# Kernel optimization log

Measured on AMD Instinct MI355X. Metric: run time of the kernel, lower is better.

Reference implementation:

```python
import jax, jax.numpy as jnp
import numpy as np

B, N, E = 16, 5000, 160000
IN, OUT, H = 64, 64, 1  # heads=1 (GATConv default)
NEG_SLOPE = 0.2


def setup_inputs() -> dict:
    key = jax.random.key(0)
    ks = jax.random.split(key, 10)
    data = jax.random.normal(ks[0], (B, N, IN), jnp.float32)
    # random edges with no self-loops (PyG removes then re-adds self-loops;
    # with no pre-existing self-loops this matches exactly)
    src = jax.random.randint(ks[1], (E,), 0, N)
    off = jax.random.randint(ks[2], (E,), 1, N)
    dst = (src + off) % N
    edge_index = jnp.stack([src, dst]).astype(jnp.int32)
    edge_attr = jax.random.uniform(ks[3], (E,), jnp.float32)
    # GATConv parameters (glorot-ish init)
    W = jax.random.normal(ks[4], (H * OUT, IN), jnp.float32) / np.sqrt(IN)
    W_edge = jax.random.normal(ks[5], (H * OUT, 1), jnp.float32)
    att_src = jax.random.normal(ks[6], (1, H, OUT), jnp.float32) * 0.1
    att_dst = jax.random.normal(ks[7], (1, H, OUT), jnp.float32) * 0.1
    att_edge = jax.random.normal(ks[8], (1, H, OUT), jnp.float32) * 0.1
    bias = jnp.zeros((H * OUT,), jnp.float32)
    return {"data": data, "edge_index": edge_index, "edge_attr": edge_attr,
            "W": W, "W_edge": W_edge, "att_src": att_src, "att_dst": att_dst,
            "att_edge": att_edge, "bias": bias}


def reference(data, edge_index, edge_attr, W, W_edge, att_src, att_dst, att_edge, bias):
    BN = B * N
    x = data.reshape(BN, IN)
    # faithful to source: tile edges per batch WITHOUT node offset
    ei = jnp.tile(edge_index, (1, B))          # [2, B*E]
    ea = jnp.tile(edge_attr, B)[:, None]        # [B*E, 1]
    # add self-loops for all BN nodes, edge_attr filled with mean
    loops = jnp.arange(BN, dtype=ei.dtype)
    src = jnp.concatenate([ei[0], loops])       # [Etot]
    dst = jnp.concatenate([ei[1], loops])
    ea = jnp.concatenate([ea, jnp.full((BN, 1), ea.mean(), ea.dtype)])
    # linear transforms
    xl = (x @ W.T).reshape(BN, H, OUT)          # [BN, H, C]
    a_src = (xl * att_src).sum(-1)              # [BN, H]
    a_dst = (xl * att_dst).sum(-1)
    e_emb = (ea @ W_edge.T).reshape(-1, H, OUT) # [Etot, H, C]
    a_edge = (e_emb * att_edge).sum(-1)         # [Etot, H]
    # per-edge attention + segment softmax over destination nodes
    alpha = a_src[src] + a_dst[dst] + a_edge
    alpha = jax.nn.leaky_relu(alpha, NEG_SLOPE)
    amax = jax.ops.segment_max(alpha, dst, num_segments=BN)
    alpha = jnp.exp(alpha - amax[dst])
    denom = jax.ops.segment_sum(alpha, dst, num_segments=BN)
    alpha = alpha / (denom[dst] + 1e-16)
    # message passing: gather src features, weight, scatter-sum to dst
    msg = xl[src] * alpha[:, :, None]           # [Etot, H, C]
    out = jax.ops.segment_sum(msg, dst, num_segments=BN)
    out = out.reshape(BN, H * OUT) + bias
    return out.reshape(B, N, OUT), jnp.stack([src, dst]), alpha
```

## Files before the change

### kernel.cpp

```cpp
#include <hip/hip_runtime.h>

#define NN 5000
#define EE 160000
#define BB 16
#define BNN 80000
#define BEE 2560000
#define ETOT 2640000
#define CAP 128
#define POISON ((int)0xAAAAAAAA)

#define GEMM_BLKS 1250
#define SUM_BLKS  80
#define OUT1_BLKS 2578
#define FILL_BLKS 625
#define MEGA_BLKS (GEMM_BLKS + SUM_BLKS + OUT1_BLKS + FILL_BLKS)

typedef __attribute__((ext_vector_type(8))) short short8;
typedef __attribute__((ext_vector_type(4))) float floatx4;

__device__ __forceinline__ short8 pack_bf8(const float* p) {
    union { unsigned int u[4]; short8 s; } r;
    #pragma unroll
    for (int j = 0; j < 4; ++j) {
        unsigned int lo = __float_as_uint(p[2 * j]) >> 16;
        unsigned int hi = __float_as_uint(p[2 * j + 1]) & 0xFFFF0000u;
        r.u[j] = lo | hi;
    }
    return r.s;
}

__global__ __launch_bounds__(256) void k_mega(
        const float* __restrict__ x, const float* __restrict__ W,
        const float* __restrict__ att_src, const float* __restrict__ att_dst,
        const float* __restrict__ bias,
        const float* __restrict__ ea, const float* __restrict__ wedge,
        const float* __restrict__ atte, const int* __restrict__ ei,
        float* __restrict__ xl, float* __restrict__ asrc, float* __restrict__ adst,
        float* __restrict__ out0,
        int* __restrict__ cursor, int* __restrict__ bucket,
        float* __restrict__ partials, float* __restrict__ out1) {
    __shared__ float red[256];
    const int blk = blockIdx.x;
    const int t = threadIdx.x;

    if (blk < GEMM_BLKS) {
        const int wave = t >> 6;
        const int lane = t & 63;
        const int quad = lane >> 4;
        const int col  = lane & 15;
        short8 bfrag[4][2];
        float attsv[4], attdv[4], biasv[4];
        #pragma unroll
        for (int ct = 0; ct < 4; ++ct) {
            int c = ct * 16 + col;
            #pragma unroll
            for (int ks = 0; ks < 2; ++ks)
                bfrag[ct][ks] = pack_bf8(W + c * 64 + ks * 32 + quad * 8);
            attsv[ct] = att_src[c];
            attdv[ct] = att_dst[c];
            biasv[ct] = bias[c];
        }
        int node0 = (blk * 4 + wave) << 4;
        short8 afrag[2];
        const float* xrow = x + (size_t)(node0 + col) * 64;
        #pragma unroll
        for (int ks = 0; ks < 2; ++ks)
            afrag[ks] = pack_bf8(xrow + ks * 32 + quad * 8);
        floatx4 acc[4];
        #pragma unroll
        for (int ct = 0; ct < 4; ++ct) acc[ct] = (floatx4){0.f, 0.f, 0.f, 0.f};
        #pragma unroll
        for (int ks = 0; ks < 2; ++ks)
            #pragma unroll
            for (int ct = 0; ct < 4; ++ct)
                acc[ct] = __builtin_amdgcn_mfma_f32_16x16x32_bf16(afrag[ks], bfrag[ct][ks], acc[ct], 0, 0, 0);
        float ps[4] = {0.f,0.f,0.f,0.f}, pd[4] = {0.f,0.f,0.f,0.f};
        #pragma unroll
        for (int r = 0; r < 4; ++r) {
            int node = node0 + quad * 4 + r;
            #pragma unroll
            for (int ct = 0; ct < 4; ++ct) {
                float v = acc[ct][r];
                out0[node * 64 + ct * 16 + col] = v + biasv[ct];
                if (node < NN) xl[node * 64 + ct * 16 + col] = v;
                ps[r] += v * attsv[ct];
                pd[r] += v * attdv[ct];
            }
        }
        #pragma unroll
        for (int off = 1; off < 16; off <<= 1) {
            #pragma unroll
            for (int r = 0; r < 4; ++r) {
                ps[r] += __shfl_xor(ps[r], off, 64);
                pd[r] += __shfl_xor(pd[r], off, 64);
            }
        }
        if (col == 0) {
            #pragma unroll
            for (int r = 0; r < 4; ++r) {
                int node = node0 + quad * 4 + r;
                if (node < NN) { asrc[node] = ps[r]; adst[node] = pd[r]; }
            }
        }
    } else if (blk < GEMM_BLKS + SUM_BLKS) {
        int sb = blk - GEMM_BLKS;
        int gid = sb * 256 + t;
        float v = 0.f;
        for (int i = gid; i < EE; i += SUM_BLKS * 256) v += ea[i];
        red[t] = v;
        __syncthreads();
        #pragma unroll
        for (int off = 128; off > 0; off >>= 1) {
            if (t < off) red[t] += red[t + off];
            __syncthreads();
        }
        if (t == 0) partials[sb] = red[0];
        if (sb == 0 && t < 64) {
            float s = wedge[t] * atte[t];
            #pragma unroll
            for (int off = 32; off > 0; off >>= 1) s += __shfl_xor(s, off, 64);
            if (t == 0) partials[80] = s;
        }
    } else if (blk < GEMM_BLKS + SUM_BLKS + OUT1_BLKS) {
        int qb = blk - (GEMM_BLKS + SUM_BLKS);
        for (int q = qb * 256 + t; q < ETOT / 4; q += OUT1_BLKS * 256) {
            int i = q * 4;
            float4 sv, dv;
            if (i < BEE) {
                int oe = i % EE;
                int4 s4 = *reinterpret_cast<const int4*>(ei + oe);
                int4 d4 = *reinterpret_cast<const int4*>(ei + EE + oe);
                sv = make_float4((float)s4.x, (float)s4.y, (float)s4.z, (float)s4.w);
                dv = make_float4((float)d4.x, (float)d4.y, (float)d4.z, (float)d4.w);
            } else {
                int nn = i - BEE;
                sv = make_float4((float)nn, (float)(nn+1), (float)(nn+2), (float)(nn+3));
                dv = sv;
            }
            *reinterpret_cast<float4*>(out1 + i) = sv;
            *reinterpret_cast<float4*>(out1 + ETOT + i) = dv;
        }
    } else {
        int fb = blk - (GEMM_BLKS + SUM_BLKS + OUT1_BLKS);
        int e = fb * 256 + t;
        int d = ei[EE + e];
        int pos = atomicAdd(&cursor[d], 1) - POISON;
        if (pos < CAP) bucket[d * CAP + pos] = e;
    }
}

__global__ __launch_bounds__(256) void k_gather(
        const int* __restrict__ ei, const float* __restrict__ ea,
        const int* __restrict__ bucket, const int* __restrict__ cursor,
        const float* __restrict__ asrc, const float* __restrict__ adst,
        const float* __restrict__ partials,
        const float* __restrict__ xl, const float* __restrict__ bias,
        float* __restrict__ albuf, float* __restrict__ selfal,
        float* __restrict__ out0) {
    __shared__ float s_r[4][CAP];
    __shared__ int   s_se[4][CAP];
    __shared__ int   s_e[4][CAP];
    int wave = threadIdx.x >> 6, lane = threadIdx.x & 63;
    int d = blockIdx.x * 4 + wave;
    int deg = min(cursor[d] - POISON, CAP);
    float s0 = 0.f;
    #pragma unroll
    for (int i = 0; i < 80; ++i) s0 += partials[i];
    float s1 = partials[80];
    float mean = s0 * (1.0f / EE);
    float ad = adst[d];
    float rs = asrc[d] + ad + mean * s1;
    rs = (rs > 0.f) ? rs : 0.2f * rs;
    float rmax = rs;
    for (int base = 0; base < deg; base += 64) {
        int idx = base + lane;
        if (idx < deg) {
            int e  = bucket[d * CAP + idx];
            int se = ei[e];
            float r = asrc[se] + ad + ea[e] * s1;
            r = (r > 0.f) ? r : 0.2f * r;
            s_r[wave][idx] = r; s_se[wave][idx] = se; s_e[wave][idx] = e;
            rmax = fmaxf(rmax, r);
        }
    }
    #pragma unroll
    for (int off = 32; off > 0; off >>= 1) rmax = fmaxf(rmax, __shfl_xor(rmax, off, 64));
    float m = rmax;
    float es = __expf(rs - m);
    float l = es;
    float acc = es * xl[d * 64 + lane];
    int j = 0;
    for (; j + 4 <= deg; j += 4) {
        int se0 = s_se[wave][j],     se1 = s_se[wave][j + 1];
        int se2 = s_se[wave][j + 2], se3 = s_se[wave][j + 3];
        float x0 = xl[se0 * 64 + lane], x1 = xl[se1 * 64 + lane];
        float x2 = xl[se2 * 64 + lane], x3 = xl[se3 * 64 + lane];
        float w0 = __expf(s_r[wave][j]     - m), w1 = __expf(s_r[wave][j + 1] - m);
        float w2 = __expf(s_r[wave][j + 2] - m), w3 = __expf(s_r[wave][j + 3] - m);
        acc += 16.0f * (w0 * x0 + w1 * x1 + w2 * x2 + w3 * x3);
        l   += 16.0f * (w0 + w1 + w2 + w3);
    }
    for (; j < deg; ++j) {
        int se0 = s_se[wave][j];
        float w0 = __expf(s_r[wave][j] - m);
        acc += 16.0f * w0 * xl[se0 * 64 + lane];
        l   += 16.0f * w0;
    }
    float inv = 1.0f / (l + 1e-16f);
    out0[d * 64 + lane] = acc * inv + bias[lane];
    if (lane == 0) selfal[d] = es * inv;
    for (int idx = lane; idx < deg; idx += 64)
        albuf[s_e[wave][idx]] = __expf(s_r[wave][idx] - m) * inv;
}

__global__ void k_alpha(const float* __restrict__ albuf,
                        const float* __restrict__ selfal,
                        float* __restrict__ out2) {
    int t = threadIdx.x;
    for (int q = blockIdx.x * 256 + t; q < ETOT / 4; q += OUT1_BLKS * 256) {
        int i = q * 4;
        float4 av;
        if (i < BEE) {
            av = *reinterpret_cast<const float4*>(albuf + (i % EE));
        } else {
            float a[4];
            #pragma unroll
            for (int jj = 0; jj < 4; ++jj) {
                int nn = i + jj - BEE;
                a[jj] = (nn < NN) ? selfal[nn] : 1.0f;
            }
            av = make_float4(a[0], a[1], a[2], a[3]);
        }
        *reinterpret_cast<float4*>(out2 + i) = av;
    }
}

extern "C" void kernel_launch(void* const* d_in, const int* in_sizes, int n_in,
                              void* d_out, int out_size, void* d_ws, size_t ws_size,
                              hipStream_t stream) {
    const float* data  = (const float*)d_in[0];
    const int*   ei    = (const int*)d_in[1];
    const float* ea    = (const float*)d_in[2];
    const float* W     = (const float*)d_in[3];
    const float* wedge = (const float*)d_in[4];
    const float* atts  = (const float*)d_in[5];
    const float* attd  = (const float*)d_in[6];
    const float* atte  = (const float*)d_in[7];
    const float* bias  = (const float*)d_in[8];

    float* out0 = (float*)d_out;
    float* out1 = out0 + 5120000;
    float* out2 = out0 + 10400000;

    float* ws = (float*)d_ws;
    float* xl       = ws;
    float* asrc     = ws + 320000;
    float* adst     = ws + 325000;
    float* albuf    = ws + 330000;
    float* selfal   = ws + 490000;
    float* partials = ws + 495000;
    int*   cursor   = (int*)(ws + 495082);
    int*   bucket   = (int*)(ws + 500082);

    k_mega  <<<MEGA_BLKS, 256, 0, stream>>>(data, W, atts, attd, bias, ea, wedge,
                                            atte, ei, xl, asrc, adst, out0,
                                            cursor, bucket, partials, out1);
    k_gather<<<1250,      256, 0, stream>>>(ei, ea, bucket, cursor, asrc, adst,
                                            partials, xl, bias, albuf, selfal, out0);
    k_alpha <<<OUT1_BLKS, 256, 0, stream>>>(albuf, selfal, out2);
}
```

Baseline: 127.5 us.

## Rebalance kernel stages: move high-node GEMM and index output into gather kernel

Measured after the change: 130.1 us. +2.1%, slower.

```diff
diff --git a/kernel.cpp b/kernel.cpp
--- a/kernel.cpp
+++ b/kernel.cpp
@@ -2,18 +2,23 @@
 
 #define NN 5000
 #define EE 160000
-#define BB 16
 #define BNN 80000
 #define BEE 2560000
 #define ETOT 2640000
 #define CAP 128
 #define POISON ((int)0xAAAAAAAA)
 
-#define GEMM_BLKS 1250
-#define SUM_BLKS  80
-#define OUT1_BLKS 2578
-#define FILL_BLKS 625
-#define MEGA_BLKS (GEMM_BLKS + SUM_BLKS + OUT1_BLKS + FILL_BLKS)
+#define K1_FILL 625
+#define K1_GEMM 79
+#define K1_SUM  80
+#define K1_BLKS (K1_FILL + K1_GEMM + K1_SUM)
+
+#define K2_GATHER 1250
+#define K2_GEMMHI 1172
+#define K2_OUT1   2578
+#define K2_BLKS   (K2_GATHER + K2_GEMMHI + K2_OUT1)
+
+#define K3_BLKS 1290
 
 typedef __attribute__((ext_vector_type(8))) short short8;
 typedef __attribute__((ext_vector_type(4))) float floatx4;
@@ -29,84 +34,113 @@
     return r.s;
 }
 
-__global__ __launch_bounds__(256) void k_mega(
+template <bool LO>
+__device__ __forceinline__ void gemm_tile(
+        int gblk, int t,
         const float* __restrict__ x, const float* __restrict__ W,
         const float* __restrict__ att_src, const float* __restrict__ att_dst,
         const float* __restrict__ bias,
+        float* __restrict__ xl, float* __restrict__ asrc, float* __restrict__ adst,
+        float* __restrict__ out0) {
+    const int wave = t >> 6;
+    const int lane = t & 63;
+    const int quad = lane >> 4;
+    const int col  = lane & 15;
+    short8 bfrag[4][2];
+    float attsv[4], attdv[4], biasv[4];
+    #pragma unroll
+    for (int ct = 0; ct < 4; ++ct) {
+        int c = ct * 16 + col;
+        #pragma unroll
+        for (int ks = 0; ks < 2; ++ks)
+            bfrag[ct][ks] = pack_bf8(W + c * 64 + ks * 32 + quad * 8);
+        if (LO) { attsv[ct] = att_src[c]; attdv[ct] = att_dst[c]; }
+        else    { biasv[ct] = bias[c]; }
+    }
+    int node0 = (gblk * 4 + wave) << 4;
+    short8 afrag[2];
+    const float* xrow = x + (size_t)(node0 + col) * 64;
+    #pragma unroll
+    for (int ks = 0; ks < 2; ++ks)
+        afrag[ks] = pack_bf8(xrow + ks * 32 + quad * 8);
+    floatx4 acc[4];
+    #pragma unroll
+    for (int ct = 0; ct < 4; ++ct) acc[ct] = (floatx4){0.f, 0.f, 0.f, 0.f};
+    #pragma unroll
+    for (int ks = 0; ks < 2; ++ks)
+        #pragma unroll
+        for (int ct = 0; ct < 4; ++ct)
+            acc[ct] = __builtin_amdgcn_mfma_f32_16x16x32_bf16(afrag[ks], bfrag[ct][ks], acc[ct], 0, 0, 0);
+    if (LO) {
+        float ps[4] = {0.f,0.f,0.f,0.f}, pd[4] = {0.f,0.f,0.f,0.f};
+        #pragma unroll
+        for (int r = 0; r < 4; ++r) {
+            int node = node0 + quad * 4 + r;
+            #pragma unroll
+            for (int ct = 0; ct < 4; ++ct) {
+                float v = acc[ct][r];
+                if (node < NN) xl[node * 64 + ct * 16 + col] = v;
+                ps[r] += v * attsv[ct];
+                pd[r] += v * attdv[ct];
+            }
+        }
+        #pragma unroll
+        for (int off = 1; off < 16; off <<= 1) {
+            #pragma unroll
+            for (int r = 0; r < 4; ++r) {
+                ps[r] += __shfl_xor(ps[r], off, 64);
+                pd[r] += __shfl_xor(pd[r], off, 64);
+            }
+        }
+        if (col == 0) {
+            #pragma unroll
+            for (int r = 0; r < 4; ++r) {
+                int node = node0 + quad * 4 + r;
+                if (node < NN) { asrc[node] = ps[r]; adst[node] = pd[r]; }
+            }
+        }
+    } else {
+        #pragma unroll
+        for (int r = 0; r < 4; ++r) {
+            int node = node0 + quad * 4 + r;
+            #pragma unroll
+            for (int ct = 0; ct < 4; ++ct) {
+                float v = acc[ct][r];
+                if (node >= NN) out0[node * 64 + ct * 16 + col] = v + biasv[ct];
+            }
+        }
+    }
+}
+
+__global__ __launch_bounds__(256) void k1(
+        const float* __restrict__ x, const float* __restrict__ W,
+        const float* __restrict__ att_src, const float* __restrict__ att_dst,
         const float* __restrict__ ea, const float* __restrict__ wedge,
         const float* __restrict__ atte, const int* __restrict__ ei,
         float* __restrict__ xl, float* __restrict__ asrc, float* __restrict__ adst,
-        float* __restrict__ out0,
-        int* __restrict__ cursor, int* __restrict__ bucket,
-        float* __restrict__ partials, float* __restrict__ out1) {
+        int* __restrict__ cursor, int* __restrict__ bucket, float* __restrict__ eabuf,
+        float* __restrict__ partials) {
     __shared__ float red[256];
     const int blk = blockIdx.x;
     const int t = threadIdx.x;
-
-    if (blk < GEMM_BLKS) {
-        const int wave = t >> 6;
-        const int lane = t & 63;
-        const int quad = lane >> 4;
-        const int col  = lane & 15;
-        short8 bfrag[4][2];
-        float attsv[4], attdv[4], biasv[4];
-        #pragma unroll
-        for (int ct = 0; ct < 4; ++ct) {
-            int c = ct * 16 + col;
-            #pragma unroll
-            for (int ks = 0; ks < 2; ++ks)
-                bfrag[ct][ks] = pack_bf8(W + c * 64 + ks * 32 + quad * 8);
-            attsv[ct] = att_src[c];
-            attdv[ct] = att_dst[c];
-            biasv[ct] = bias[c];
-        }
-        int node0 = (blk * 4 + wave) << 4;
-        short8 afrag[2];
-        const float* xrow = x + (size_t)(node0 + col) * 64;
-        #pragma unroll
-        for (int ks = 0; ks < 2; ++ks)
-            afrag[ks] = pack_bf8(xrow + ks * 32 + quad * 8);
-        floatx4 acc[4];
-        #pragma unroll
-        for (int ct = 0; ct < 4; ++ct) acc[ct] = (floatx4){0.f, 0.f, 0.f, 0.f};
-        #pragma unroll
-        for (int ks = 0; ks < 2; ++ks)
-            #pragma unroll
-            for (int ct = 0; ct < 4; ++ct)
-                acc[ct] = __builtin_amdgcn_mfma_f32_16x16x32_bf16(afrag[ks], bfrag[ct][ks], acc[ct], 0, 0, 0);
-        float ps[4] = {0.f,0.f,0.f,0.f}, pd[4] = {0.f,0.f,0.f,0.f};
-        #pragma unroll
-        for (int r = 0; r < 4; ++r) {
-            int node = node0 + quad * 4 + r;
-            #pragma unroll
-            for (int ct = 0; ct < 4; ++ct) {
-                float v = acc[ct][r];
-                out0[node * 64 + ct * 16 + col] = v + biasv[ct];
-                if (node < NN) xl[node * 64 + ct * 16 + col] = v;
-                ps[r] += v * attsv[ct];
-                pd[r] += v * attdv[ct];
-            }
-        }
-        #pragma unroll
-        for (int off = 1; off < 16; off <<= 1) {
-            #pragma unroll
-            for (int r = 0; r < 4; ++r) {
-                ps[r] += __shfl_xor(ps[r], off, 64);
-                pd[r] += __shfl_xor(pd[r], off, 64);
-            }
-        }
-        if (col == 0) {
-            #pragma unroll
-            for (int r = 0; r < 4; ++r) {
-                int node = node0 + quad * 4 + r;
-                if (node < NN) { asrc[node] = ps[r]; adst[node] = pd[r]; }
-            }
-        }
-    } else if (blk < GEMM_BLKS + SUM_BLKS) {
-        int sb = blk - GEMM_BLKS;
+    if (blk < K1_FILL) {
+        int e = blk * 256 + t;
+        int s = ei[e];
+        int d = ei[EE + e];
+        float ev = ea[e];
+        int pos = atomicAdd(&cursor[d], 1) - POISON;
+        if (pos < CAP) {
+            bucket[d * CAP + pos] = (s << 18) | e;
+            eabuf[d * CAP + pos] = ev;
+        }
+    } else if (blk < K1_FILL + K1_GEMM) {
+        gemm_tile<true>(blk - K1_FILL, t, x, W, att_src, att_dst, nullptr,
+                        xl, asrc, adst, nullptr);
+    } else {
+        int sb = blk - (K1_FILL + K1_GEMM);
         int gid = sb * 256 + t;
         float v = 0.f;
-        for (int i = gid; i < EE; i += SUM_BLKS * 256) v += ea[i];
+        for (int i = gid; i < EE; i += K1_SUM * 256) v += ea[i];
         red[t] = v;
         __syncthreads();
         #pragma unroll
@@ -121,9 +155,85 @@
             for (int off = 32; off > 0; off >>= 1) s += __shfl_xor(s, off, 64);
             if (t == 0) partials[80] = s;
         }
-    } else if (blk < GEMM_BLKS + SUM_BLKS + OUT1_BLKS) {
-        int qb = blk - (GEMM_BLKS + SUM_BLKS);
-        for (int q = qb * 256 + t; q < ETOT / 4; q += OUT1_BLKS * 256) {
+    }
+}
+
+__global__ __launch_bounds__(256) void k2(
+        const float* __restrict__ x, const float* __restrict__ W,
+        const float* __restrict__ bias,
+        const int* __restrict__ ei,
+        const int* __restrict__ bucket, const float* __restrict__ eabuf,
+        const int* __restrict__ cursor,
+        const float* __restrict__ asrc, const float* __restrict__ adst,
+        const float* __restrict__ partials,
+        const float* __restrict__ xl,
+        float* __restrict__ albuf, float* __restrict__ selfal,
+        float* __restrict__ out0, float* __restrict__ out1) {
+    __shared__ float s_r[4][CAP];
+    __shared__ int   s_se[4][CAP];
+    __shared__ int   s_e[4][CAP];
+    const int blk = blockIdx.x;
+    const int t = threadIdx.x, w = t >> 6, lane = t & 63;
+
+    if (blk < K2_GATHER) {
+        float s0 = 0.f;
+        #pragma unroll
+        for (int i = 0; i < 80; ++i) s0 += partials[i];
+        float s1 = partials[80];
+        float selfadd = s0 * (1.0f / EE) * s1;
+        float bl = bias[lane];
+        int d = blk * 4 + w;
+        float* sr = s_r[w]; int* sse = s_se[w]; int* se_ = s_e[w];
+        int deg = min(cursor[d] - POISON, CAP);
+        float ad = adst[d];
+        float rs = asrc[d] + ad + selfadd;
+        rs = (rs > 0.f) ? rs : 0.2f * rs;
+        float rmax = rs;
+        for (int base = 0; base < deg; base += 64) {
+            int idx = base + lane;
+            if (idx < deg) {
+                int packed = bucket[d * CAP + idx];
+                float ev   = eabuf[d * CAP + idx];
+                int se = packed >> 18;
+                int e  = packed & 0x3FFFF;
+                float r = asrc[se] + ad + ev * s1;
+                r = (r > 0.f) ? r : 0.2f * r;
+                sr[idx] = r; sse[idx] = se; se_[idx] = e;
+                rmax = fmaxf(rmax, r);
+            }
+        }
+        #pragma unroll
+        for (int off = 32; off > 0; off >>= 1) rmax = fmaxf(rmax, __shfl_xor(rmax, off, 64));
+        float m = rmax;
+        float es = __expf(rs - m);
+        float l = es;
+        float acc = es * xl[d * 64 + lane];
+        int j = 0;
+        for (; j + 4 <= deg; j += 4) {
+            int a0 = sse[j], a1 = sse[j + 1], a2 = sse[j + 2], a3 = sse[j + 3];
+            float x0 = xl[a0 * 64 + lane], x1 = xl[a1 * 64 + lane];
+            float x2 = xl[a2 * 64 + lane], x3 = xl[a3 * 64 + lane];
+            float w0 = __expf(sr[j] - m),     w1 = __expf(sr[j + 1] - m);
+            float w2 = __expf(sr[j + 2] - m), w3 = __expf(sr[j + 3] - m);
+            acc += 16.0f * (w0 * x0 + w1 * x1 + w2 * x2 + w3 * x3);
+            l   += 16.0f * (w0 + w1 + w2 + w3);
+        }
+        for (; j < deg; ++j) {
+            float w0 = __expf(sr[j] - m);
+            acc += 16.0f * w0 * xl[sse[j] * 64 + lane];
+            l   += 16.0f * w0;
+        }
+        float inv = 1.0f / (l + 1e-16f);
+        out0[d * 64 + lane] = acc * inv + bl;
+        if (lane == 0) selfal[d] = es * inv;
+        for (int idx = lane; idx < deg; idx += 64)
+            albuf[se_[idx]] = __expf(sr[idx] - m) * inv;
+    } else if (blk < K2_GATHER + K2_GEMMHI) {
+        gemm_tile<false>(78 + (blk - K2_GATHER), t, x, W, nullptr, nullptr, bias,
+                         nullptr, nullptr, nullptr, out0);
+    } else {
+        int qb = blk - (K2_GATHER + K2_GEMMHI);
+        for (int q = qb * 256 + t; q < ETOT / 4; q += K2_OUT1 * 256) {
             int i = q * 4;
             float4 sv, dv;
             if (i < BEE) {
@@ -140,84 +250,13 @@
             *reinterpret_cast<float4*>(out1 + i) = sv;
             *reinterpret_cast<float4*>(out1 + ETOT + i) = dv;
         }
-    } else {
-        int fb = blk - (GEMM_BLKS + SUM_BLKS + OUT1_BLKS);
-        int e = fb * 256 + t;
-        int d = ei[EE + e];
-        int pos = atomicAdd(&cursor[d], 1) - POISON;
-        if (pos < CAP) bucket[d * CAP + pos] = e;
-    }
-}
-
-__global__ __launch_bounds__(256) void k_gather(
-        const int* __restrict__ ei, const float* __restrict__ ea,
-        const int* __restrict__ bucket, const int* __restrict__ cursor,
-        const float* __restrict__ asrc, const float* __restrict__ adst,
-        const float* __restrict__ partials,
-        const float* __restrict__ xl, const float* __restrict__ bias,
-        float* __restrict__ albuf, float* __restrict__ selfal,
-        float* __restrict__ out0) {
-    __shared__ float s_r[4][CAP];
-    __shared__ int   s_se[4][CAP];
-    __shared__ int   s_e[4][CAP];
-    int wave = threadIdx.x >> 6, lane = threadIdx.x & 63;
-    int d = blockIdx.x * 4 + wave;
-    int deg = min(cursor[d] - POISON, CAP);
-    float s0 = 0.f;
-    #pragma unroll
-    for (int i = 0; i < 80; ++i) s0 += partials[i];
-    float s1 = partials[80];
-    float mean = s0 * (1.0f / EE);
-    float ad = adst[d];
-    float rs = asrc[d] + ad + mean * s1;
-    rs = (rs > 0.f) ? rs : 0.2f * rs;
-    float rmax = rs;
-    for (int base = 0; base < deg; base += 64) {
-        int idx = base + lane;
-        if (idx < deg) {
-            int e  = bucket[d * CAP + idx];
-            int se = ei[e];
-            float r = asrc[se] + ad + ea[e] * s1;
-            r = (r > 0.f) ? r : 0.2f * r;
-            s_r[wave][idx] = r; s_se[wave][idx] = se; s_e[wave][idx] = e;
-            rmax = fmaxf(rmax, r);
-        }
-    }
-    #pragma unroll
-    for (int off = 32; off > 0; off >>= 1) rmax = fmaxf(rmax, __shfl_xor(rmax, off, 64));
-    float m = rmax;
-    float es = __expf(rs - m);
-    float l = es;
-    float acc = es * xl[d * 64 + lane];
-    int j = 0;
-    for (; j + 4 <= deg; j += 4) {
-        int se0 = s_se[wave][j],     se1 = s_se[wave][j + 1];
-        int se2 = s_se[wave][j + 2], se3 = s_se[wave][j + 3];
-        float x0 = xl[se0 * 64 + lane], x1 = xl[se1 * 64 + lane];
-        float x2 = xl[se2 * 64 + lane], x3 = xl[se3 * 64 + lane];
-        float w0 = __expf(s_r[wave][j]     - m), w1 = __expf(s_r[wave][j + 1] - m);
-        float w2 = __expf(s_r[wave][j + 2] - m), w3 = __expf(s_r[wave][j + 3] - m);
-        acc += 16.0f * (w0 * x0 + w1 * x1 + w2 * x2 + w3 * x3);
-        l   += 16.0f * (w0 + w1 + w2 + w3);
-    }
-    for (; j < deg; ++j) {
-        int se0 = s_se[wave][j];
-        float w0 = __expf(s_r[wave][j] - m);
-        acc += 16.0f * w0 * xl[se0 * 64 + lane];
-        l   += 16.0f * w0;
-    }
-    float inv = 1.0f / (l + 1e-16f);
-    out0[d * 64 + lane] = acc * inv + bias[lane];
-    if (lane == 0) selfal[d] = es * inv;
-    for (int idx = lane; idx < deg; idx += 64)
-        albuf[s_e[wave][idx]] = __expf(s_r[wave][idx] - m) * inv;
-}
-
-__global__ void k_alpha(const float* __restrict__ albuf,
-                        const float* __restrict__ selfal,
-                        float* __restrict__ out2) {
-    int t = threadIdx.x;
-    for (int q = blockIdx.x * 256 + t; q < ETOT / 4; q += OUT1_BLKS * 256) {
+    }
+}
+
+__global__ __launch_bounds__(256) void k3(
+        const float* __restrict__ albuf, const float* __restrict__ selfal,
+        float* __restrict__ out2) {
+    for (int q = blockIdx.x * 256 + threadIdx.x; q < ETOT / 4; q += K3_BLKS * 256) {
         int i = q * 4;
         float4 av;
         if (i < BEE) {
@@ -242,11 +281,11 @@
     const int*   ei    = (const int*)d_in[1];
     const float* ea    = (const float*)d_in[2];
     const float* W     = (const float*)d_in[3];
-    const float* wedge = (const float*)d_in[4];
     const float* atts  = (const float*)d_in[5];
     const float* attd  = (const float*)d_in[6];
     const float* atte  = (const float*)d_in[7];
     const float* bias  = (const float*)d_in[8];
+    const float* wedge = (const float*)d_in[4];
 
     float* out0 = (float*)d_out;
     float* out1 = out0 + 5120000;
@@ -261,11 +300,12 @@
     float* partials = ws + 495000;
     int*   cursor   = (int*)(ws + 495082);
     int*   bucket   = (int*)(ws + 500082);
-
-    k_mega  <<<MEGA_BLKS, 256, 0, stream>>>(data, W, atts, attd, bias, ea, wedge,
-                                            atte, ei, xl, asrc, adst, out0,
-                                            cursor, bucket, partials, out1);
-    k_gather<<<1250,      256, 0, stream>>>(ei, ea, bucket, cursor, asrc, adst,
-                                            partials, xl, bias, albuf, selfal, out0);
-    k_alpha <<<OUT1_BLKS, 256, 0, stream>>>(albuf, selfal, out2);
-}
+    float* eabuf    = ws + 1140082;
+
+    k1<<<K1_BLKS, 256, 0, stream>>>(data, W, atts, attd, ea, wedge, atte, ei,
+                                    xl, asrc, adst, cursor, bucket, eabuf, partials);
+    k2<<<K2_BLKS, 256, 0, stream>>>(data, W, bias, ei, bucket, eabuf, cursor,
+                                    asrc, adst, partials, xl,
+                                    albuf, selfal, out0, out1);
+    k3<<<K3_BLKS, 256, 0, stream>>>(albuf, selfal, out2);
+}
```
